# Performance work log

Measured on AMD Instinct MI355X. Metric: run time of the kernel, lower is better.

The kernel has to match this reference:

```python
import jax, jax.numpy as jnp
import numpy as np

N_NODES = 100000
N_EDGES = 1200000
N_GRAPHS = 8
IN_DIM = 64
HID = 64
N_CLASSES = 2


def setup_inputs() -> dict:
    key = jax.random.key(0)
    ks = jax.random.split(key, 8)
    features = jax.random.normal(ks[0], (N_NODES, IN_DIM), dtype=jnp.float32)
    W1 = jax.random.normal(ks[1], (IN_DIM, HID), dtype=jnp.float32) * (1.0 / np.sqrt(IN_DIM))
    b1 = jnp.zeros((HID,), dtype=jnp.float32)
    W2 = jax.random.normal(ks[2], (HID, HID), dtype=jnp.float32) * (1.0 / np.sqrt(HID))
    b2 = jnp.zeros((HID,), dtype=jnp.float32)
    Wp = jax.random.normal(ks[3], (HID, N_CLASSES), dtype=jnp.float32) * (1.0 / np.sqrt(HID))
    bp = jnp.zeros((N_CLASSES,), dtype=jnp.float32)
    edge_src = jax.random.randint(ks[4], (N_EDGES,), 0, N_NODES, dtype=jnp.int64 if jax.config.jax_enable_x64 else jnp.int32)
    edge_dst = jax.random.randint(ks[5], (N_EDGES,), 0, N_NODES, dtype=edge_src.dtype)
    graph_id = jnp.sort(jax.random.randint(ks[6], (N_NODES,), 0, N_GRAPHS, dtype=edge_src.dtype))
    return {"features": features, "W1": W1, "b1": b1, "W2": W2, "b2": b2,
            "Wp": Wp, "bp": bp, "edge_src": edge_src, "edge_dst": edge_dst,
            "graph_id": graph_id}


def reference(features, W1, b1, W2, b2, Wp, bp, edge_src, edge_dst, graph_id):
    N = features.shape[0]
    dt = features.dtype
    ones_e = jnp.ones(edge_src.shape[0], dtype=dt)
    # DGL GraphConv norm='both': symmetric normalization with out-deg (src) / in-deg (dst)
    out_deg = jnp.clip(jax.ops.segment_sum(ones_e, edge_src, num_segments=N), 1.0)
    in_deg = jnp.clip(jax.ops.segment_sum(ones_e, edge_dst, num_segments=N), 1.0)
    src_norm = jax.lax.rsqrt(out_deg)[:, None]  # [N,1]
    dst_norm = jax.lax.rsqrt(in_deg)[:, None]   # [N,1]

    def gconv(h, W, b):
        h = h * src_norm
        msgs = h[edge_src]                                    # [E, d] gather
        agg = jax.ops.segment_sum(msgs, edge_dst, num_segments=N)  # [N, d]
        agg = agg * dst_norm
        return jax.nn.relu(agg @ W + b)

    h = gconv(features, W1, b1)   # [N, HID]
    h = gconv(h, W2, b2)          # [N, HID]

    # dgl.mean_nodes: per-graph mean pooling
    cnt = jnp.clip(jax.ops.segment_sum(jnp.ones(N, dtype=dt), graph_id, num_segments=N_GRAPHS), 1.0)
    hg = jax.ops.segment_sum(h, graph_id, num_segments=N_GRAPHS) / cnt[:, None]  # [G, HID]
    return hg @ Wp + bp
```

## Files before the change

### kernel.cpp

```cpp
#include <hip/hip_runtime.h>

#define NN 100000
#define NE 1200000
#define NG 8
#define DIM 64
#define WROW 64
#define SCAN_BS 256
#define NB ((NN + SCAN_BS - 1) / SCAN_BS)
#define COLCAP (NE + 7 * NN)

#define RANGE 16384
#define RSH 14
#define NR 7
#define GSL 28
#define SLICE4 ((NE / 4 + GSL - 1) / GSL)

__global__ __launch_bounds__(256) void hist_kernel(const int4* __restrict__ esrc4,
                                                   const int4* __restrict__ edst4,
                                                   int* __restrict__ partial) {
  __shared__ int h[RANGE];
  int job = blockIdx.x;
  int g = job % GSL;
  int r = (job / GSL) % NR;
  int dir = job / (GSL * NR);
  const int4* __restrict__ idx = dir ? edst4 : esrc4;
  int lo = r * RANGE, hi = min(lo + RANGE, NN);
  for (int i = threadIdx.x; i < RANGE / 4; i += 256) ((int4*)h)[i] = make_int4(0, 0, 0, 0);
  __syncthreads();
  int s0 = g * SLICE4, s1 = min(s0 + SLICE4, NE / 4);
  for (int i = s0 + threadIdx.x; i < s1; i += 256) {
    int4 v = idx[i];
    if (v.x >= lo && v.x < hi) atomicAdd(&h[v.x - lo], 1);
    if (v.y >= lo && v.y < hi) atomicAdd(&h[v.y - lo], 1);
    if (v.z >= lo && v.z < hi) atomicAdd(&h[v.z - lo], 1);
    if (v.w >= lo && v.w < hi) atomicAdd(&h[v.w - lo], 1);
  }
  __syncthreads();
  int4* dst = (int4*)(partial + (size_t)job * RANGE);
  int cap4 = (hi - lo) >> 2;
  for (int i = threadIdx.x; i < cap4; i += 256) dst[i] = ((int4*)h)[i];
}

__global__ void reduce_kernel(const int* __restrict__ partial, int* __restrict__ indeg,
                              float* __restrict__ snormA, float* __restrict__ dnormA, int N) {
  int t = blockIdx.x * blockDim.x + threadIdx.x;
  if (t >= 2 * N) return;
  int dir = t >= N;
  int n = dir ? t - N : t;
  int r = n >> RSH, off = n & (RANGE - 1);
  const int* p = partial + (((size_t)dir * NR + r) * GSL) * RANGE + off;
  int s = 0;
#pragma unroll
  for (int g = 0; g < GSL; ++g) s += p[(size_t)g * RANGE];
  float nv = rsqrtf(fmaxf((float)s, 1.0f));
  if (dir) { indeg[n] = s; dnormA[n] = nv; }
  else snormA[n] = nv;
}

__global__ __launch_bounds__(SCAN_BS) void scan1_kernel(const int* __restrict__ indeg,
                                                        int* __restrict__ rp2,
                                                        int* __restrict__ bsum, int N) {
  __shared__ int t[SCAN_BS];
  int i = blockIdx.x * SCAN_BS + threadIdx.x;
  int v = (i < N) ? ((indeg[i] + 7) & ~7) : 0;
  t[threadIdx.x] = v;
  __syncthreads();
  for (int off = 1; off < SCAN_BS; off <<= 1) {
    int u = (threadIdx.x >= off) ? t[threadIdx.x - off] : 0;
    __syncthreads();
    t[threadIdx.x] += u;
    __syncthreads();
  }
  if (i < N) rp2[i] = t[threadIdx.x] - v;
  if (i == N - 1) rp2[N] = t[threadIdx.x];
  if (threadIdx.x == SCAN_BS - 1) bsum[blockIdx.x] = t[threadIdx.x];
}

__global__ __launch_bounds__(512) void scan2_kernel(const int* __restrict__ bsum,
                                                    int* __restrict__ boff, int nb) {
  __shared__ int t[512];
  int v = ((int)threadIdx.x < nb) ? bsum[threadIdx.x] : 0;
  t[threadIdx.x] = v;
  __syncthreads();
  for (int off = 1; off < 512; off <<= 1) {
    int u = (threadIdx.x >= off) ? t[threadIdx.x - off] : 0;
    __syncthreads();
    t[threadIdx.x] += u;
    __syncthreads();
  }
  boff[threadIdx.x] = t[threadIdx.x] - v;
}

__global__ __launch_bounds__(SCAN_BS) void scan3_kernel(int* __restrict__ rp2,
                                                        const int* __restrict__ boff, int N) {
  int i = blockIdx.x * SCAN_BS + threadIdx.x;
  if (i < N) rp2[i] += boff[blockIdx.x];
  if (i == N - 1) rp2[N] += boff[blockIdx.x];
}

__global__ void offscan_kernel(int* __restrict__ partial, const int* __restrict__ rp2, int N) {
  int n = blockIdx.x * blockDim.x + threadIdx.x;
  if (n >= N) return;
  int r = n >> RSH, i = n & (RANGE - 1);
  int* p = partial + (((size_t)NR + r) * GSL) * RANGE + i;
  int running = rp2[n];
#pragma unroll
  for (int g = 0; g < GSL; ++g) {
    int tmp = p[(size_t)g * RANGE];
    p[(size_t)g * RANGE] = running;
    running += tmp;
  }
}

__global__ void colinit_kernel(int4* __restrict__ col4, int n4) {
  int i = blockIdx.x * blockDim.x + threadIdx.x;
  int st = gridDim.x * blockDim.x;
  for (; i < n4; i += st) col4[i] = make_int4(NN, NN, NN, NN);
}

__global__ __launch_bounds__(256) void fill_kernel(const int4* __restrict__ esrc4,
                                                   const int4* __restrict__ edst4,
                                                   const int* __restrict__ partial,
                                                   int* __restrict__ col) {
  __shared__ int cnt[RANGE];
  int job = blockIdx.x;
  int g = job % GSL, r = job / GSL;
  int lo = r * RANGE, hi = min(lo + RANGE, NN);
  const int* off = partial + (((size_t)NR + r) * GSL + g) * RANGE;
  for (int i = threadIdx.x; i < hi - lo; i += 256) cnt[i] = off[i];
  __syncthreads();
  int s0 = g * SLICE4, s1 = min(s0 + SLICE4, NE / 4);
  for (int i = s0 + threadIdx.x; i < s1; i += 256) {
    int4 d = edst4[i];
    int4 s = esrc4[i];
    if (d.x >= lo && d.x < hi) col[atomicAdd(&cnt[d.x - lo], 1)] = s.x;
    if (d.y >= lo && d.y < hi) col[atomicAdd(&cnt[d.y - lo], 1)] = s.y;
    if (d.z >= lo && d.z < hi) col[atomicAdd(&cnt[d.z - lo], 1)] = s.z;
    if (d.w >= lo && d.w < hi) col[atomicAdd(&cnt[d.w - lo], 1)] = s.w;
  }
}

__global__ void prescale_kernel(const float* __restrict__ f, const float* __restrict__ snormA,
                                float* __restrict__ xs, int N) {
  int i = blockIdx.x * blockDim.x + threadIdx.x;
  if (i < N * 16) {
    int n = i >> 4;
    float sn = snormA[n];
    float4 v = ((const float4*)f)[i];
    v.x *= sn; v.y *= sn; v.z *= sn; v.w *= sn;
    ((float4*)xs)[i] = v;
  }
}

template <int POOL>
__global__ __launch_bounds__(256) void gconv_kernel(
    const float* __restrict__ xs, const float* __restrict__ snormA, const float* __restrict__ dnormA,
    const int* __restrict__ rp2, const int* __restrict__ col,
    const float* __restrict__ W, const float* __restrict__ b,
    float* __restrict__ out, const int* __restrict__ gid,
    float* __restrict__ gsum, float* __restrict__ gcnt, int N) {
  __shared__ float Wt[DIM * WROW];
  __shared__ float aL[4][4][DIM];
  __shared__ float lsum[NG * DIM];
  __shared__ float lcnt[NG];
  for (int i = threadIdx.x; i < DIM * 16; i += 256) {
    int k = i >> 4, ch = i & 15;
    *(float4*)&Wt[k * WROW + ch * 4] = *(const float4*)(W + k * DIM + ch * 4);
  }
  if (POOL) {
    for (int i = threadIdx.x; i < NG * DIM; i += 256) lsum[i] = 0.0f;
    if (threadIdx.x < NG) lcnt[threadIdx.x] = 0.0f;
  }
  __syncthreads();

  const int lane = threadIdx.x & 63;
  const int wid = threadIdx.x >> 6;
  const int g = lane >> 4;
  const int idx = lane & 15;
  const int t4 = idx << 2;
  const float4 bb = *(const float4*)(b + t4);
  const int waveId = blockIdx.x * 4 + wid;
  const int stride4 = gridDim.x * 16;

  for (int n4 = waveId * 4; n4 < N; n4 += stride4) {
    int n = n4 + g;
    bool valid = n < N;
    int nc = valid ? n : 0;
    int base = rp2[nc];
    int end = rp2[nc + 1];
    float4 acc = make_float4(0.f, 0.f, 0.f, 0.f);
    float4 acc2 = make_float4(0.f, 0.f, 0.f, 0.f);
    for (int p = base; p < end; p += 8) {
      int4 c0 = *(const int4*)(col + p);
      int4 c1 = *(const int4*)(col + p + 4);
      float4 v0 = *(const float4*)(xs + (size_t)c0.x * DIM + t4);
      float4 v1 = *(const float4*)(xs + (size_t)c0.y * DIM + t4);
      float4 v2 = *(const float4*)(xs + (size_t)c0.z * DIM + t4);
      float4 v3 = *(const float4*)(xs + (size_t)c0.w * DIM + t4);
      float4 v4 = *(const float4*)(xs + (size_t)c1.x * DIM + t4);
      float4 v5 = *(const float4*)(xs + (size_t)c1.y * DIM + t4);
      float4 v6 = *(const float4*)(xs + (size_t)c1.z * DIM + t4);
      float4 v7 = *(const float4*)(xs + (size_t)c1.w * DIM + t4);
      acc.x += (v0.x + v1.x) + (v2.x + v3.x);
      acc.y += (v0.y + v1.y) + (v2.y + v3.y);
      acc.z += (v0.z + v1.z) + (v2.z + v3.z);
      acc.w += (v0.w + v1.w) + (v2.w + v3.w);
      acc2.x += (v4.x + v5.x) + (v6.x + v7.x);
      acc2.y += (v4.y + v5.y) + (v6.y + v7.y);
      acc2.z += (v4.z + v5.z) + (v6.z + v7.z);
      acc2.w += (v4.w + v5.w) + (v6.w + v7.w);
    }
    float dn = dnormA[nc];
    acc.x = (acc.x + acc2.x) * dn;
    acc.y = (acc.y + acc2.y) * dn;
    acc.z = (acc.z + acc2.z) * dn;
    acc.w = (acc.w + acc2.w) * dn;

    *(float4*)&aL[wid][g][t4] = acc;

    float4 r = bb;
#pragma unroll
    for (int kc = 0; kc < 16; ++kc) {
      float4 av = *(const float4*)&aL[wid][g][4 * kc];
      float4 w0 = *(const float4*)(Wt + (4 * kc + 0) * WROW + t4);
      float4 w1 = *(const float4*)(Wt + (4 * kc + 1) * WROW + t4);
      float4 w2 = *(const float4*)(Wt + (4 * kc + 2) * WROW + t4);
      float4 w3 = *(const float4*)(Wt + (4 * kc + 3) * WROW + t4);
      r.x = fmaf(av.x, w0.x, r.x); r.y = fmaf(av.x, w0.y, r.y);
      r.z = fmaf(av.x, w0.z, r.z); r.w = fmaf(av.x, w0.w, r.w);
      r.x = fmaf(av.y, w1.x, r.x); r.y = fmaf(av.y, w1.y, r.y);
      r.z = fmaf(av.y, w1.z, r.z); r.w = fmaf(av.y, w1.w, r.w);
      r.x = fmaf(av.z, w2.x, r.x); r.y = fmaf(av.z, w2.y, r.y);
      r.z = fmaf(av.z, w2.z, r.z); r.w = fmaf(av.z, w2.w, r.w);
      r.x = fmaf(av.w, w3.x, r.x); r.y = fmaf(av.w, w3.y, r.y);
      r.z = fmaf(av.w, w3.z, r.z); r.w = fmaf(av.w, w3.w, r.w);
    }
    r.x = fmaxf(r.x, 0.f); r.y = fmaxf(r.y, 0.f);
    r.z = fmaxf(r.z, 0.f); r.w = fmaxf(r.w, 0.f);

    if (POOL) {
      if (valid) {
        int gi = gid[n];
        atomicAdd(&lsum[gi * DIM + t4 + 0], r.x);
        atomicAdd(&lsum[gi * DIM + t4 + 1], r.y);
        atomicAdd(&lsum[gi * DIM + t4 + 2], r.z);
        atomicAdd(&lsum[gi * DIM + t4 + 3], r.w);
        if (idx == 0) atomicAdd(&lcnt[gi], 1.0f);
      }
    } else if (valid) {
      float sn = snormA[n];
      float4 o = make_float4(r.x * sn, r.y * sn, r.z * sn, r.w * sn);
      *(float4*)(out + (size_t)n * DIM + t4) = o;
    }
  }

  if (POOL) {
    __syncthreads();
    for (int i = threadIdx.x; i < NG * DIM; i += 256) atomicAdd(&gsum[i], lsum[i]);
    if (threadIdx.x < NG) atomicAdd(&gcnt[threadIdx.x], lcnt[threadIdx.x]);
  }
}

__global__ void final_kernel(const float* __restrict__ gsum, const float* __restrict__ gcnt,
                             const float* __restrict__ Wp, const float* __restrict__ bp,
                             float* __restrict__ out) {
  int lane = threadIdx.x;
#pragma unroll
  for (int g = 0; g < NG; ++g) {
    float inv = 1.0f / fmaxf(gcnt[g], 1.0f);
    float hv = gsum[g * DIM + lane] * inv;
#pragma unroll
    for (int c = 0; c < 2; ++c) {
      float p = hv * Wp[lane * 2 + c];
      for (int off = 32; off; off >>= 1) p += __shfl_down(p, off, 64);
      if (lane == 0) out[g * 2 + c] = p + bp[c];
    }
  }
}

extern "C" void kernel_launch(void* const* d_in, const int* in_sizes, int n_in,
                              void* d_out, int out_size, void* d_ws, size_t ws_size,
                              hipStream_t stream) {
  const float* features = (const float*)d_in[0];
  const float* W1 = (const float*)d_in[1];
  const float* b1 = (const float*)d_in[2];
  const float* W2 = (const float*)d_in[3];
  const float* b2 = (const float*)d_in[4];
  const float* Wp = (const float*)d_in[5];
  const float* bp = (const float*)d_in[6];
  const int* esrc = (const int*)d_in[7];
  const int* edst = (const int*)d_in[8];
  const int* gid = (const int*)d_in[9];
  float* out = (float*)d_out;

  const int N = NN;

  float* base = (float*)d_ws;
  size_t off = 0;
  auto alloc = [&](size_t nwords) { size_t r = off; off = (off + nwords + 15) & ~(size_t)15; return r; };

  float* gsum = base + alloc(NG * DIM);
  float* gcnt = base + alloc(NG);
  size_t zeroWords = off;
  int* indeg  = (int*)(base + alloc(N));
  float* snormA = base + alloc(N);
  float* dnormA = base + alloc(N);
  int* rp2   = (int*)(base + alloc(N + 1));
  int* bsum  = (int*)(base + alloc(512));
  int* boff  = (int*)(base + alloc(512));
  int* col   = (int*)(base + alloc(COLCAP));
  float* xs  = base + alloc((size_t)(N + 1) * DIM);
  float* B   = base + alloc((size_t)(N + 1) * DIM);
  int* partial = (int*)xs;

  hipMemsetAsync(d_ws, 0, zeroWords * sizeof(float), stream);
  hipMemsetAsync(B + (size_t)N * DIM, 0, DIM * sizeof(float), stream);

  hist_kernel<<<2 * NR * GSL, 256, 0, stream>>>((const int4*)esrc, (const int4*)edst, partial);
  reduce_kernel<<<(2 * N + 255) / 256, 256, 0, stream>>>(partial, indeg, snormA, dnormA, N);

  scan1_kernel<<<NB, SCAN_BS, 0, stream>>>(indeg, rp2, bsum, N);
  scan2_kernel<<<1, 512, 0, stream>>>(bsum, boff, NB);
  scan3_kernel<<<NB, SCAN_BS, 0, stream>>>(rp2, boff, N);

  offscan_kernel<<<(NR * RANGE + 255) / 256, 256, 0, stream>>>(partial, rp2, N);
  colinit_kernel<<<(COLCAP / 4 + 255) / 256, 256, 0, stream>>>((int4*)col, COLCAP / 4);
  fill_kernel<<<NR * GSL, 256, 0, stream>>>((const int4*)esrc, (const int4*)edst, partial, col);

  hipMemsetAsync(xs + (size_t)N * DIM, 0, DIM * sizeof(float), stream);
  prescale_kernel<<<(N * 16 + 255) / 256, 256, 0, stream>>>(features, snormA, xs, N);

  gconv_kernel<0><<<2048, 256, 0, stream>>>(xs, snormA, dnormA, rp2, col, W1, b1,
                                            B, gid, gsum, gcnt, N);
  gconv_kernel<1><<<2048, 256, 0, stream>>>(B, snormA, dnormA, rp2, col, W2, b2,
                                            nullptr, gid, gsum, gcnt, N);

  final_kernel<<<1, 64, 0, stream>>>(gsum, gcnt, Wp, bp, out);
}
```

Measured before the change: 246.3 us.

## Fuse degree reduction into scan and fold source norm into first gather

Removes the separate reduce kernel by summing the per-slice degree histograms directly inside the first scan pass, which writes both norm arrays. It also drops the prescale pass over the features. The first graph conv now gathers raw features and applies the source norm per edge, with padding indices clamped and given a zero weight. This saves one full read/write of the feature matrix and two launches. In exchange the first gather does an extra scalar load per edge, and the partial histogram buffer now gets its own workspace instead of aliasing xs.

```diff
diff --git a/kernel.cpp b/kernel.cpp
--- a/kernel.cpp
+++ b/kernel.cpp
@@ -41,28 +41,28 @@
   for (int i = threadIdx.x; i < cap4; i += 256) dst[i] = ((int4*)h)[i];
 }
 
-__global__ void reduce_kernel(const int* __restrict__ partial, int* __restrict__ indeg,
-                              float* __restrict__ snormA, float* __restrict__ dnormA, int N) {
-  int t = blockIdx.x * blockDim.x + threadIdx.x;
-  if (t >= 2 * N) return;
-  int dir = t >= N;
-  int n = dir ? t - N : t;
-  int r = n >> RSH, off = n & (RANGE - 1);
-  const int* p = partial + (((size_t)dir * NR + r) * GSL) * RANGE + off;
-  int s = 0;
-#pragma unroll
-  for (int g = 0; g < GSL; ++g) s += p[(size_t)g * RANGE];
-  float nv = rsqrtf(fmaxf((float)s, 1.0f));
-  if (dir) { indeg[n] = s; dnormA[n] = nv; }
-  else snormA[n] = nv;
-}
-
-__global__ __launch_bounds__(SCAN_BS) void scan1_kernel(const int* __restrict__ indeg,
+__global__ __launch_bounds__(SCAN_BS) void scan1_kernel(const int* __restrict__ partial,
+                                                        float* __restrict__ snormA,
+                                                        float* __restrict__ dnormA,
                                                         int* __restrict__ rp2,
                                                         int* __restrict__ bsum, int N) {
   __shared__ int t[SCAN_BS];
   int i = blockIdx.x * SCAN_BS + threadIdx.x;
-  int v = (i < N) ? ((indeg[i] + 7) & ~7) : 0;
+  int v = 0;
+  if (i < N) {
+    int r = i >> RSH, off = i & (RANGE - 1);
+    const int* ps = partial + ((size_t)r * GSL) * RANGE + off;
+    const int* pd = partial + (((size_t)NR + r) * GSL) * RANGE + off;
+    int sOut = 0, sIn = 0;
+#pragma unroll
+    for (int g = 0; g < GSL; ++g) {
+      sOut += ps[(size_t)g * RANGE];
+      sIn += pd[(size_t)g * RANGE];
+    }
+    snormA[i] = rsqrtf(fmaxf((float)sOut, 1.0f));
+    dnormA[i] = rsqrtf(fmaxf((float)sIn, 1.0f));
+    v = (sIn + 7) & ~7;
+  }
   t[threadIdx.x] = v;
   __syncthreads();
   for (int off = 1; off < SCAN_BS; off <<= 1) {
@@ -140,19 +140,7 @@
   }
 }
 
-__global__ void prescale_kernel(const float* __restrict__ f, const float* __restrict__ snormA,
-                                float* __restrict__ xs, int N) {
-  int i = blockIdx.x * blockDim.x + threadIdx.x;
-  if (i < N * 16) {
-    int n = i >> 4;
-    float sn = snormA[n];
-    float4 v = ((const float4*)f)[i];
-    v.x *= sn; v.y *= sn; v.z *= sn; v.w *= sn;
-    ((float4*)xs)[i] = v;
-  }
-}
-
-template <int POOL>
+template <int PRESCALED, int POOL>
 __global__ __launch_bounds__(256) void gconv_kernel(
     const float* __restrict__ xs, const float* __restrict__ snormA, const float* __restrict__ dnormA,
     const int* __restrict__ rp2, const int* __restrict__ col,
@@ -193,22 +181,47 @@
     for (int p = base; p < end; p += 8) {
       int4 c0 = *(const int4*)(col + p);
       int4 c1 = *(const int4*)(col + p + 4);
-      float4 v0 = *(const float4*)(xs + (size_t)c0.x * DIM + t4);
-      float4 v1 = *(const float4*)(xs + (size_t)c0.y * DIM + t4);
-      float4 v2 = *(const float4*)(xs + (size_t)c0.z * DIM + t4);
-      float4 v3 = *(const float4*)(xs + (size_t)c0.w * DIM + t4);
-      float4 v4 = *(const float4*)(xs + (size_t)c1.x * DIM + t4);
-      float4 v5 = *(const float4*)(xs + (size_t)c1.y * DIM + t4);
-      float4 v6 = *(const float4*)(xs + (size_t)c1.z * DIM + t4);
-      float4 v7 = *(const float4*)(xs + (size_t)c1.w * DIM + t4);
-      acc.x += (v0.x + v1.x) + (v2.x + v3.x);
-      acc.y += (v0.y + v1.y) + (v2.y + v3.y);
-      acc.z += (v0.z + v1.z) + (v2.z + v3.z);
-      acc.w += (v0.w + v1.w) + (v2.w + v3.w);
-      acc2.x += (v4.x + v5.x) + (v6.x + v7.x);
-      acc2.y += (v4.y + v5.y) + (v6.y + v7.y);
-      acc2.z += (v4.z + v5.z) + (v6.z + v7.z);
-      acc2.w += (v4.w + v5.w) + (v6.w + v7.w);
+      if (PRESCALED) {
+        float4 v0 = *(const float4*)(xs + (size_t)c0.x * DIM + t4);
+        float4 v1 = *(const float4*)(xs + (size_t)c0.y * DIM + t4);
+        float4 v2 = *(const float4*)(xs + (size_t)c0.z * DIM + t4);
+        float4 v3 = *(const float4*)(xs + (size_t)c0.w * DIM + t4);
+        float4 v4 = *(const float4*)(xs + (size_t)c1.x * DIM + t4);
+        float4 v5 = *(const float4*)(xs + (size_t)c1.y * DIM + t4);
+        float4 v6 = *(const float4*)(xs + (size_t)c1.z * DIM + t4);
+        float4 v7 = *(const float4*)(xs + (size_t)c1.w * DIM + t4);
+        acc.x += (v0.x + v1.x) + (v2.x + v3.x);
+        acc.y += (v0.y + v1.y) + (v2.y + v3.y);
+        acc.z += (v0.z + v1.z) + (v2.z + v3.z);
+        acc.w += (v0.w + v1.w) + (v2.w + v3.w);
+        acc2.x += (v4.x + v5.x) + (v6.x + v7.x);
+        acc2.y += (v4.y + v5.y) + (v6.y + v7.y);
+        acc2.z += (v4.z + v5.z) + (v6.z + v7.z);
+        acc2.w += (v4.w + v5.w) + (v6.w + v7.w);
+      } else {
+        float w0 = snormA[c0.x], w1 = snormA[c0.y], w2 = snormA[c0.z], w3 = snormA[c0.w];
+        float w4 = snormA[c1.x], w5 = snormA[c1.y], w6 = snormA[c1.z], w7 = snormA[c1.w];
+        int s0 = min(c0.x, NN - 1), s1 = min(c0.y, NN - 1);
+        int s2 = min(c0.z, NN - 1), s3 = min(c0.w, NN - 1);
+        int s4 = min(c1.x, NN - 1), s5 = min(c1.y, NN - 1);
+        int s6 = min(c1.z, NN - 1), s7 = min(c1.w, NN - 1);
+        float4 v0 = *(const float4*)(xs + (size_t)s0 * DIM + t4);
+        float4 v1 = *(const float4*)(xs + (size_t)s1 * DIM + t4);
+        float4 v2 = *(const float4*)(xs + (size_t)s2 * DIM + t4);
+        float4 v3 = *(const float4*)(xs + (size_t)s3 * DIM + t4);
+        float4 v4 = *(const float4*)(xs + (size_t)s4 * DIM + t4);
+        float4 v5 = *(const float4*)(xs + (size_t)s5 * DIM + t4);
+        float4 v6 = *(const float4*)(xs + (size_t)s6 * DIM + t4);
+        float4 v7 = *(const float4*)(xs + (size_t)s7 * DIM + t4);
+        acc.x = fmaf(v0.x, w0, fmaf(v1.x, w1, fmaf(v2.x, w2, fmaf(v3.x, w3, acc.x))));
+        acc.y = fmaf(v0.y, w0, fmaf(v1.y, w1, fmaf(v2.y, w2, fmaf(v3.y, w3, acc.y))));
+        acc.z = fmaf(v0.z, w0, fmaf(v1.z, w1, fmaf(v2.z, w2, fmaf(v3.z, w3, acc.z))));
+        acc.w = fmaf(v0.w, w0, fmaf(v1.w, w1, fmaf(v2.w, w2, fmaf(v3.w, w3, acc.w))));
+        acc2.x = fmaf(v4.x, w4, fmaf(v5.x, w5, fmaf(v6.x, w6, fmaf(v7.x, w7, acc2.x))));
+        acc2.y = fmaf(v4.y, w4, fmaf(v5.y, w5, fmaf(v6.y, w6, fmaf(v7.y, w7, acc2.y))));
+        acc2.z = fmaf(v4.z, w4, fmaf(v5.z, w5, fmaf(v6.z, w6, fmaf(v7.z, w7, acc2.z))));
+        acc2.w = fmaf(v4.w, w4, fmaf(v5.w, w5, fmaf(v6.w, w6, fmaf(v7.w, w7, acc2.w))));
+      }
     }
     float dn = dnormA[nc];
     acc.x = (acc.x + acc2.x) * dn;
@@ -294,6 +307,7 @@
   float* out = (float*)d_out;
 
   const int N = NN;
+  const size_t NPART = (size_t)2 * NR * GSL * RANGE;
 
   float* base = (float*)d_ws;
   size_t off = 0;
@@ -302,24 +316,22 @@
   float* gsum = base + alloc(NG * DIM);
   float* gcnt = base + alloc(NG);
   size_t zeroWords = off;
-  int* indeg  = (int*)(base + alloc(N));
-  float* snormA = base + alloc(N);
+  float* snormA = base + alloc(N + 1);
   float* dnormA = base + alloc(N);
   int* rp2   = (int*)(base + alloc(N + 1));
   int* bsum  = (int*)(base + alloc(512));
   int* boff  = (int*)(base + alloc(512));
   int* col   = (int*)(base + alloc(COLCAP));
-  float* xs  = base + alloc((size_t)(N + 1) * DIM);
+  int* partial = (int*)(base + alloc(NPART));
   float* B   = base + alloc((size_t)(N + 1) * DIM);
-  int* partial = (int*)xs;
 
   hipMemsetAsync(d_ws, 0, zeroWords * sizeof(float), stream);
+  hipMemsetAsync(snormA + N, 0, sizeof(float), stream);
   hipMemsetAsync(B + (size_t)N * DIM, 0, DIM * sizeof(float), stream);
 
   hist_kernel<<<2 * NR * GSL, 256, 0, stream>>>((const int4*)esrc, (const int4*)edst, partial);
-  reduce_kernel<<<(2 * N + 255) / 256, 256, 0, stream>>>(partial, indeg, snormA, dnormA, N);
-
-  scan1_kernel<<<NB, SCAN_BS, 0, stream>>>(indeg, rp2, bsum, N);
+
+  scan1_kernel<<<NB, SCAN_BS, 0, stream>>>(partial, snormA, dnormA, rp2, bsum, N);
   scan2_kernel<<<1, 512, 0, stream>>>(bsum, boff, NB);
   scan3_kernel<<<NB, SCAN_BS, 0, stream>>>(rp2, boff, N);
 
@@ -327,13 +339,10 @@
   colinit_kernel<<<(COLCAP / 4 + 255) / 256, 256, 0, stream>>>((int4*)col, COLCAP / 4);
   fill_kernel<<<NR * GSL, 256, 0, stream>>>((const int4*)esrc, (const int4*)edst, partial, col);
 
-  hipMemsetAsync(xs + (size_t)N * DIM, 0, DIM * sizeof(float), stream);
-  prescale_kernel<<<(N * 16 + 255) / 256, 256, 0, stream>>>(features, snormA, xs, N);
-
-  gconv_kernel<0><<<2048, 256, 0, stream>>>(xs, snormA, dnormA, rp2, col, W1, b1,
-                                            B, gid, gsum, gcnt, N);
-  gconv_kernel<1><<<2048, 256, 0, stream>>>(B, snormA, dnormA, rp2, col, W2, b2,
-                                            nullptr, gid, gsum, gcnt, N);
+  gconv_kernel<0, 0><<<2048, 256, 0, stream>>>(features, snormA, dnormA, rp2, col, W1, b1,
+                                               B, gid, gsum, gcnt, N);
+  gconv_kernel<1, 1><<<2048, 256, 0, stream>>>(B, snormA, dnormA, rp2, col, W2, b2,
+                                               nullptr, gid, gsum, gcnt, N);
 
   final_kernel<<<1, 64, 0, stream>>>(gsum, gcnt, Wp, bp, out);
 }
```

After: 247.9 us. No clear change (+0.6%).
